# Performance work log

Measured on AMD Instinct MI355X. Metric: run time of the kernel, lower is better.

Reference implementation:

```python
import jax, jax.numpy as jnp
import numpy as np

D_MODEL = 1024
NUM_HEADS = 16
D_K = D_MODEL // NUM_HEADS
FFN_SIZE = 4096
EPS = 1e-6


def _layer_norm(x, gamma, beta):
    mu = jnp.mean(x, axis=-1, keepdims=True)
    var = jnp.var(x, axis=-1, keepdims=True)
    return (x - mu) / jnp.sqrt(var + EPS) * gamma + beta


def setup_inputs() -> dict:
    key = jax.random.key(0)
    ks = jax.random.split(key, 12)
    B, S = 2, 2048
    s_attn = 1.0 / np.sqrt(D_MODEL)
    s_ffn1 = 1.0 / np.sqrt(D_MODEL)
    s_ffn2 = 1.0 / np.sqrt(FFN_SIZE)
    return {
        "x": jax.random.normal(ks[0], (B, S, D_MODEL), dtype=jnp.float32),
        "W_q": jax.random.normal(ks[1], (D_MODEL, D_MODEL), dtype=jnp.float32) * s_attn,
        "W_k": jax.random.normal(ks[2], (D_MODEL, D_MODEL), dtype=jnp.float32) * s_attn,
        "W_v": jax.random.normal(ks[3], (D_MODEL, D_MODEL), dtype=jnp.float32) * s_attn,
        "W_o": jax.random.normal(ks[4], (D_MODEL, D_MODEL), dtype=jnp.float32) * s_attn,
        "b_o": jnp.zeros((D_MODEL,), dtype=jnp.float32),
        "W1": jax.random.normal(ks[5], (D_MODEL, FFN_SIZE), dtype=jnp.float32) * s_ffn1,
        "b1": jnp.zeros((FFN_SIZE,), dtype=jnp.float32),
        "W2": jax.random.normal(ks[6], (FFN_SIZE, D_MODEL), dtype=jnp.float32) * s_ffn2,
        "b2": jnp.zeros((D_MODEL,), dtype=jnp.float32),
        "ln1_g": jnp.ones((D_MODEL,), dtype=jnp.float32),
        "ln1_b": jnp.zeros((D_MODEL,), dtype=jnp.float32),
        "ln2_g": jnp.ones((D_MODEL,), dtype=jnp.float32),
        "ln2_b": jnp.zeros((D_MODEL,), dtype=jnp.float32),
    }


def reference(x, W_q, W_k, W_v, W_o, b_o, W1, b1, W2, b2,
              ln1_g, ln1_b, ln2_g, ln2_b):
    B, S, _ = x.shape

    # --- self-attention sublayer (pre-norm residual) ---
    h = _layer_norm(x, ln1_g, ln1_b)
    q = (h @ W_q).reshape(B, S, NUM_HEADS, D_K).transpose(0, 2, 1, 3)  # [B,H,S,Dk]
    k = (h @ W_k).reshape(B, S, NUM_HEADS, D_K).transpose(0, 2, 1, 3)
    v = (h @ W_v).reshape(B, S, NUM_HEADS, D_K).transpose(0, 2, 1, 3)
    scores = jnp.einsum("bhqd,bhkd->bhqk", q, k) / jnp.sqrt(jnp.float32(D_K))
    attn = jax.nn.softmax(scores, axis=-1)
    ctx = jnp.einsum("bhqk,bhkd->bhqd", attn, v)
    ctx = ctx.transpose(0, 2, 1, 3).reshape(B, S, D_MODEL)
    x = x + (ctx @ W_o + b_o)

    # --- FFN sublayer (pre-norm residual) ---
    h2 = _layer_norm(x, ln2_g, ln2_b)
    f = jax.nn.relu(h2 @ W1 + b1) @ W2 + b2
    return x + f
```

## Files before the change

kernel.cpp:

```cpp
#include <hip/hip_runtime.h>
#include <cstdint>
#include <cstddef>


typedef __attribute__((ext_vector_type(8))) __bf16 bf16x8;
typedef __attribute__((ext_vector_type(4))) __bf16 bf16x4;
typedef __attribute__((ext_vector_type(4))) float f32x4;

__device__ __forceinline__ void async16(const void* g, void* l) {
  __builtin_amdgcn_global_load_lds(
      (__attribute__((address_space(1))) void*)g,
      (__attribute__((address_space(3))) void*)l, 16, 0, 0);
}

__device__ __forceinline__ f32x4 mfma16(bf16x8 a, bf16x8 b, f32x4 c) {
  return __builtin_amdgcn_mfma_f32_16x16x32_bf16(a, b, c, 0, 0, 0);
}

template <int N>
__device__ __forceinline__ void wait_vmcnt() {
  if constexpr (N == 0) {
    asm volatile("s_waitcnt vmcnt(0)" ::: "memory");
  } else if constexpr (N == 3) {
    asm volatile("s_waitcnt vmcnt(3)" ::: "memory");
  } else {
    asm volatile("s_waitcnt vmcnt(4)" ::: "memory");
  }
}
__device__ __forceinline__ void barrier_raw() {
  asm volatile("s_barrier" ::: "memory");
}
__device__ __forceinline__ void lgkm0() {
  asm volatile("s_waitcnt lgkmcnt(0)" ::: "memory");
}

__global__ __launch_bounds__(256) void transpose_all(
    const float* __restrict__ Wq, const float* __restrict__ Wk,
    const float* __restrict__ Wv, const float* __restrict__ Wo,
    const float* __restrict__ W1, const float* __restrict__ W2,
    __bf16* __restrict__ WqkvT, __bf16* __restrict__ WoT,
    __bf16* __restrict__ W1T, __bf16* __restrict__ W2T) {
  const int id = blockIdx.x;
  const float* in;
  __bf16* out;
  int ld_in, ld_out, c0, r0;
  if (id < 1024) {
    const int which = id >> 8, tl = id & 255;
    c0 = (tl & 15) * 64;
    r0 = (tl >> 4) * 64;
    ld_in = 1024;
    ld_out = 1024;
    if (which == 0) { in = Wq; out = WqkvT; }
    else if (which == 1) { in = Wk; out = WqkvT + 1048576; }
    else if (which == 2) { in = Wv; out = WqkvT + 2097152; }
    else { in = Wo; out = WoT; }
  } else if (id < 2048) {
    const int tl = id - 1024;
    c0 = (tl & 63) * 64;
    r0 = (tl >> 6) * 64;
    in = W1; out = W1T; ld_in = 4096; ld_out = 1024;
  } else {
    const int tl = id - 2048;
    c0 = (tl & 15) * 64;
    r0 = (tl >> 4) * 64;
    in = W2; out = W2T; ld_in = 1024; ld_out = 4096;
  }
  __shared__ __bf16 tile[64][65];
  const int tx = threadIdx.x & 63, ty = threadIdx.x >> 6;
#pragma unroll
  for (int i = 0; i < 16; i++) {
    int r = ty + i * 4;
    tile[r][tx] = (__bf16)in[(size_t)(r0 + r) * ld_in + c0 + tx];
  }
  __syncthreads();
#pragma unroll
  for (int i = 0; i < 16; i++) {
    int r = ty + i * 4;
    out[(size_t)(c0 + r) * ld_out + r0 + tx] = tile[tx][r];
  }
}

__global__ __launch_bounds__(256) void transpose_vt_perm(
    const unsigned short* __restrict__ in, unsigned short* __restrict__ out,
    int ld_in, int ld_out) {
  __shared__ unsigned short tile[64][65];
  const int c0 = blockIdx.x * 64, r0 = blockIdx.y * 64;
  const int tx = threadIdx.x & 63, ty = threadIdx.x >> 6;
#pragma unroll
  for (int i = 0; i < 16; i++) {
    int r = ty + i * 4;
    tile[r][tx] = in[(size_t)(r0 + r) * ld_in + c0 + tx];
  }
  __syncthreads();
  const int ptx = (tx & 32) + 2 * (tx & 15) + ((tx >> 4) & 1);
#pragma unroll
  for (int i = 0; i < 16; i++) {
    int r = ty + i * 4;
    out[(size_t)(c0 + r) * ld_out + r0 + ptx] = tile[tx][r];
  }
}

__global__ __launch_bounds__(256) void ln_kernel(
    const float* __restrict__ xin, const float* __restrict__ g,
    const float* __restrict__ bt, __bf16* __restrict__ out) {
  const int tok = blockIdx.x * 4 + (threadIdx.x >> 6);
  const int lane = threadIdx.x & 63;
  const int base0 = lane * 8, base1 = 512 + lane * 8;
  const float* xr = xin + (size_t)tok * 1024;
  float v[16];
  float4 a0 = *(const float4*)(xr + base0);
  float4 a1 = *(const float4*)(xr + base0 + 4);
  float4 a2 = *(const float4*)(xr + base1);
  float4 a3 = *(const float4*)(xr + base1 + 4);
  v[0] = a0.x; v[1] = a0.y; v[2] = a0.z; v[3] = a0.w;
  v[4] = a1.x; v[5] = a1.y; v[6] = a1.z; v[7] = a1.w;
  v[8] = a2.x; v[9] = a2.y; v[10] = a2.z; v[11] = a2.w;
  v[12] = a3.x; v[13] = a3.y; v[14] = a3.z; v[15] = a3.w;
  float s = 0.f, s2 = 0.f;
#pragma unroll
  for (int i = 0; i < 16; i++) { s += v[i]; s2 += v[i] * v[i]; }
#pragma unroll
  for (int m = 1; m < 64; m <<= 1) {
    s += __shfl_xor(s, m);
    s2 += __shfl_xor(s2, m);
  }
  const float mean = s * (1.f / 1024.f);
  const float var = s2 * (1.f / 1024.f) - mean * mean;
  const float rstd = rsqrtf(var + 1e-6f);
  float4 g0 = *(const float4*)(g + base0), g1 = *(const float4*)(g + base0 + 4);
  float4 g2 = *(const float4*)(g + base1), g3 = *(const float4*)(g + base1 + 4);
  float4 b0 = *(const float4*)(bt + base0), b1v = *(const float4*)(bt + base0 + 4);
  float4 b2v = *(const float4*)(bt + base1), b3 = *(const float4*)(bt + base1 + 4);
  float gg[16] = {g0.x, g0.y, g0.z, g0.w, g1.x, g1.y, g1.z, g1.w,
                  g2.x, g2.y, g2.z, g2.w, g3.x, g3.y, g3.z, g3.w};
  float bb[16] = {b0.x, b0.y, b0.z, b0.w, b1v.x, b1v.y, b1v.z, b1v.w,
                  b2v.x, b2v.y, b2v.z, b2v.w, b3.x, b3.y, b3.z, b3.w};
  bf16x8 o0, o1;
#pragma unroll
  for (int j = 0; j < 8; j++) {
    o0[j] = (__bf16)((v[j] - mean) * rstd * gg[j] + bb[j]);
    o1[j] = (__bf16)((v[8 + j] - mean) * rstd * gg[8 + j] + bb[8 + j]);
  }
  __bf16* op = out + (size_t)tok * 1024;
  *(bf16x8*)(op + base0) = o0;
  *(bf16x8*)(op + base1) = o1;
}

template <int EPI, int SPLITS = 1>
__global__ __launch_bounds__(512, 2) void gemm256(
    const __bf16* __restrict__ A, int lda, const __bf16* __restrict__ BT,
    int ldb, void* __restrict__ C, int ldc, int Kb,
    const float* __restrict__ bias) {
  const int t = threadIdx.x;
  const int m0 = blockIdx.x * 256, n0 = blockIdx.y * 256;
  const int kz = (SPLITS > 1) ? blockIdx.z : 0;
  __shared__ __align__(16) __bf16 As[2][2][8192];
  __shared__ __align__(16) __bf16 Bs[2][2][8192];
  const int lane = t & 63;
  const int quad = lane >> 4, l15 = lane & 15;
  const int w = t >> 6, wm = w >> 2, wn = w & 3;

  f32x4 acc[8][4] = {};

  const int rr = t >> 3;
  const int ca = (t & 7) ^ (rr & 7);
  const int cc = rr & 31;
  const int wnb = t >> 8;
  const int cb = (t & 7) ^ (cc & 7);
  const __bf16* gA = A + (size_t)kz * Kb + (size_t)(m0 + rr) * lda + ca * 8;
  const __bf16* gB = BT + (size_t)kz * Kb +
                     (size_t)(n0 + wnb * 64 + cc) * ldb + cb * 8;
  const size_t a64 = (size_t)64 * lda, a128 = (size_t)128 * lda;
  const size_t b32 = (size_t)32 * ldb, b128 = (size_t)128 * ldb;

  auto stageA = [&](int buf, int mq, int ko) {
    const __bf16* g = gA + (mq ? a64 : 0) + ko;
    __bf16* l = &As[buf][mq][t * 8];
    async16(g, l);
    async16(g + a128, l + 4096);
  };
  auto stageB = [&](int buf, int nq, int ko) {
    const __bf16* g = gB + (nq ? b32 : 0) + ko;
    __bf16* l = &Bs[buf][nq][t * 8];
    async16(g, l);
    async16(g + b128, l + 4096);
  };

  const int arow = wm * 4096 + l15 * 64;
  const int brow = wn * 2048 + l15 * 64;
  const int x7 = l15 & 7;

  auto loadA = [&](int buf, int mq, bf16x8 (&af)[4][2]) {
#pragma unroll
    for (int mi = 0; mi < 4; mi++)
#pragma unroll
      for (int kk = 0; kk < 2; kk++)
        af[mi][kk] = *(const bf16x8*)&As[buf][mq]
            [arow + mi * 1024 + (((kk * 4 + quad) ^ x7) * 8)];
  };
  auto loadB = [&](int buf, int nq, bf16x8 (&bv)[2][2]) {
#pragma unroll
    for (int ni = 0; ni < 2; ni++)
#pragma unroll
      for (int kk = 0; kk < 2; kk++)
        bv[ni][kk] = *(const bf16x8*)&Bs[buf][nq]
            [brow + ni * 1024 + (((kk * 4 + quad) ^ x7) * 8)];
  };
  auto mm = [&](int mq, int nq, const bf16x8 (&af)[4][2],
                const bf16x8 (&bv)[2][2]) {
    __builtin_amdgcn_s_setprio(1);
#pragma unroll
    for (int mi = 0; mi < 4; mi++)
#pragma unroll
      for (int ni = 0; ni < 2; ni++)
#pragma unroll
        for (int kk = 0; kk < 2; kk++)
          acc[mq * 4 + mi][nq * 2 + ni] =
              mfma16(af[mi][kk], bv[ni][kk], acc[mq * 4 + mi][nq * 2 + ni]);
    __builtin_amdgcn_s_setprio(0);
  };

  const int NT = Kb / 64;
  stageA(0, 0, 0); stageB(0, 0, 0); stageA(0, 1, 0); stageB(0, 1, 0);
  stageA(1, 0, 64); stageB(1, 0, 64);
  wait_vmcnt<4>();
  barrier_raw();

  bf16x8 af[4][2], b0[2][2], b1[2][2];
  for (int s = 0; s < NT; ++s) {
    const int buf = s & 1;
    const int ko1 = (s + 1) * 64, ko2 = (s + 2) * 64;
    loadA(buf, 0, af);
    loadB(buf, 0, b0);
    if (s + 1 < NT) stageA(buf ^ 1, 1, ko1);
    barrier_raw();
    lgkm0();
    mm(0, 0, af, b0);
    barrier_raw();
    loadB(buf, 1, b1);
    if (s + 1 < NT) stageB(buf ^ 1, 1, ko1);
    barrier_raw();
    lgkm0();
    mm(0, 1, af, b1);
    barrier_raw();
    loadA(buf, 1, af);
    if (s + 2 < NT) stageA(buf, 0, ko2);
    barrier_raw();
    lgkm0();
    mm(1, 0, af, b0);
    barrier_raw();
    if (s + 2 < NT) {
      stageB(buf, 0, ko2);
      wait_vmcnt<4>();
    } else {
      wait_vmcnt<0>();
    }
    barrier_raw();
    mm(1, 1, af, b1);
    barrier_raw();
  }

  float biasv[4];
  if constexpr (EPI == 2) {
#pragma unroll
    for (int ni = 0; ni < 4; ni++)
      biasv[ni] = bias[n0 + wn * 64 + ni * 16 + l15];
  }
  __bf16* Cb = (__bf16*)C;
  if constexpr (SPLITS > 1)
    Cb += (size_t)kz * (size_t)gridDim.x * 256 * ldc;
#pragma unroll
  for (int mi = 0; mi < 8; mi++)
#pragma unroll
    for (int ni = 0; ni < 4; ni++)
#pragma unroll
      for (int r = 0; r < 4; r++) {
        const int row = m0 + wm * 128 + mi * 16 + quad * 4 + r;
        const int col = n0 + wn * 64 + ni * 16 + l15;
        float v = acc[mi][ni][r];
        if constexpr (EPI == 0) {
          Cb[(size_t)row * ldc + col] = (__bf16)v;
        } else {
          v += biasv[ni];
          Cb[(size_t)row * ldc + col] = (__bf16)fmaxf(v, 0.f);
        }
      }
}

template <int EPI, int TM, int SPLITS = 1>
__global__ __launch_bounds__(256) void gemm_bt(
    const __bf16* __restrict__ A, int lda, const __bf16* __restrict__ BT,
    int ldb, void* __restrict__ C, int ldc, int Kb,
    const float* __restrict__ bias, const float* __restrict__ res, int ldres) {
  const int t = threadIdx.x;
  const int m0 = blockIdx.x * TM, n0 = blockIdx.y * 128;
  const int kz = (SPLITS > 1) ? blockIdx.z : 0;
  __shared__ __align__(16) __bf16 As[3][TM * 32];
  __shared__ __align__(16) __bf16 Bs[3][128 * 32];
  const int lane = t & 63, w = t >> 6;
  const int quad = lane >> 4, l15 = lane & 15;
  const int wm = w >> 1, wn = w & 1;
  constexpr int MF = TM / 32;
  constexpr int LOADS = TM / 64 + 2;

  f32x4 acc[MF][4] = {};

  const int swc = ((t & 3) ^ ((t >> 3) & 3)) * 8;
  const __bf16* ga = A + (size_t)(m0 + (t >> 2)) * lda + swc + (size_t)kz * Kb;
  const __bf16* gb = BT + (size_t)(n0 + (t >> 2)) * ldb + swc + (size_t)kz * Kb;
  const size_t a64 = (size_t)64 * lda, b64 = (size_t)64 * ldb;

  auto stage = [&](int buf) {
#pragma unroll
    for (int i = 0; i < TM / 64; i++)
      async16(ga + i * a64, As[buf] + t * 8 + i * 2048);
    async16(gb, Bs[buf] + t * 8);
    async16(gb + b64, Bs[buf] + t * 8 + 2048);
    ga += 32;
    gb += 32;
  };
  const int ce = (quad ^ ((l15 >> 1) & 3)) * 8;
  auto compute = [&](int buf) {
    bf16x8 af[MF], bfr[4];
#pragma unroll
    for (int i = 0; i < MF; i++)
      af[i] = *(const bf16x8*)&As[buf][(wm * (TM / 2) + i * 16 + l15) * 32 + ce];
#pragma unroll
    for (int i = 0; i < 4; i++)
      bfr[i] = *(const bf16x8*)&Bs[buf][(wn * 64 + i * 16 + l15) * 32 + ce];
#pragma unroll
    for (int mi = 0; mi < MF; mi++)
#pragma unroll
      for (int ni = 0; ni < 4; ni++)
        acc[mi][ni] = mfma16(af[mi], bfr[ni], acc[mi][ni]);
  };

  const int iters = Kb / 32;
  stage(0);
  stage(1);
  int cur = 0, stg = 2;
  for (int it = 0; it < iters - 1; ++it) {
    wait_vmcnt<LOADS>();
    barrier_raw();
    if (it + 2 < iters) stage(stg);
    compute(cur);
    cur = (cur == 2) ? 0 : cur + 1;
    stg = (stg == 2) ? 0 : stg + 1;
  }
  wait_vmcnt<0>();
  barrier_raw();
  compute(cur);

  float biasv[4];
  if constexpr (EPI != 0) {
#pragma unroll
    for (int ni = 0; ni < 4; ni++)
      biasv[ni] = bias[n0 + wn * 64 + ni * 16 + l15];
  }
  __bf16* Cb = (__bf16*)C;
  if constexpr (SPLITS > 1)
    Cb += (size_t)kz * gridDim.x * TM * ldc;
#pragma unroll
  for (int mi = 0; mi < MF; mi++)
#pragma unroll
    for (int ni = 0; ni < 4; ni++)
#pragma unroll
      for (int r = 0; r < 4; r++) {
        const int row = m0 + wm * (TM / 2) + mi * 16 + quad * 4 + r;
        const int col = n0 + wn * 64 + ni * 16 + l15;
        float v = acc[mi][ni][r];
        if constexpr (EPI == 0) {
          Cb[(size_t)row * ldc + col] = (__bf16)v;
        } else if constexpr (EPI == 1) {
          v += biasv[ni] + res[(size_t)row * ldres + col];
          ((float*)C)[(size_t)row * ldc + col] = v;
        } else {
          v += biasv[ni];
          ((__bf16*)C)[(size_t)row * ldc + col] = (__bf16)fmaxf(v, 0.f);
        }
      }
}

__global__ __launch_bounds__(256) void reduce_split4(
    const __bf16* __restrict__ P, const float* __restrict__ bias,
    const float* __restrict__ res, float* __restrict__ out) {
  const int row = blockIdx.x, c = threadIdx.x * 4;
  const size_t i = (size_t)row * 1024 + c;
  float4 r = *(const float4*)(res + i);
  float4 bv = *(const float4*)(bias + c);
  float s0 = r.x + bv.x, s1 = r.y + bv.y, s2 = r.z + bv.z, s3 = r.w + bv.w;
#pragma unroll
  for (int j = 0; j < 4; j++) {
    bf16x4 p = *(const bf16x4*)(P + (size_t)j * 4194304 + i);
    s0 += (float)p[0];
    s1 += (float)p[1];
    s2 += (float)p[2];
    s3 += (float)p[3];
  }
  float4 o = {s0, s1, s2, s3};
  *(float4*)(out + i) = o;
}

__global__ __launch_bounds__(256, 2) void attn_kernel(
    const __bf16* __restrict__ QKV, const __bf16* __restrict__ VT,
    __bf16* __restrict__ ctx) {
  const int qt = blockIdx.x, bh = blockIdx.y;
  const int b = bh >> 4, h = bh & 15;
  const int t = threadIdx.x, w = t >> 6, lane = t & 63;
  const int quad = lane >> 4, l15 = lane & 15;
  const int tok0 = b * 2048;
  const int q0w = tok0 + qt * 128 + w * 32;

  __shared__ __align__(16) __bf16 Ks[2][128 * 64];
  __shared__ __align__(16) __bf16 VTs[2][64 * 128];

  const float qs = 0.18033688011112042f;
  bf16x8 qf[2][2];
#pragma unroll
  for (int mi = 0; mi < 2; mi++)
#pragma unroll
    for (int kb = 0; kb < 2; kb++) {
      const __bf16* src = QKV + (size_t)(q0w + mi * 16 + l15) * 3072 + h * 64 +
                          kb * 32 + quad * 8;
      bf16x8 r = *(const bf16x8*)src;
#pragma unroll
      for (int j = 0; j < 8; j++) r[j] = (__bf16)((float)r[j] * qs);
      qf[mi][kb] = r;
    }

  f32x4 lacc[2] = {};
  f32x4 O[2][4] = {};

  const int krow = t >> 3;
  const int kcg = (((t & 7) ^ (krow & 7)) * 8);
  const int vrow = t >> 4;
  const int vcg = (((2 * (t & 15)) ^ ((vrow & 7) * 2)) * 4);
  const int x7 = l15 & 7;

  auto stage = [&](int buf, int kt) {
    const int ktok = tok0 + kt * 128;
#pragma unroll
    for (int j = 0; j < 4; j++) {
      const __bf16* gp =
          QKV + (size_t)(ktok + krow + j * 32) * 3072 + 1024 + h * 64 + kcg;
      async16(gp, Ks[buf] + t * 8 + j * 2048);
    }
#pragma unroll
    for (int j = 0; j < 4; j++) {
      const __bf16* gp =
          VT + (size_t)(h * 64 + vrow + j * 16) * 4096 + ktok + vcg;
      async16(gp, VTs[buf] + t * 8 + j * 2048);
    }
  };

  stage(0, 0);
  wait_vmcnt<0>();
  barrier_raw();

  int buf = 0;
  for (int kt = 0; kt < 16; ++kt) {
    if (kt + 1 < 16) stage(buf ^ 1, kt + 1);

    f32x4 sT[2][8];
    __builtin_amdgcn_s_setprio(1);
#pragma unroll
    for (int kt8 = 0; kt8 < 8; kt8++) {
      f32x4 a0 = {}, a1 = {};
#pragma unroll
      for (int kb = 0; kb < 2; kb++) {
        bf16x8 kf = *(const bf16x8*)&Ks[buf][(kt8 * 16 + l15) * 64 +
                                            (((kb * 4 + quad) ^ x7) * 8)];
        a0 = mfma16(kf, qf[0][kb], a0);
        a1 = mfma16(kf, qf[1][kb], a1);
      }
      sT[0][kt8] = a0;
      sT[1][kt8] = a1;
    }
    __builtin_amdgcn_s_setprio(0);

#pragma unroll
    for (int kb = 0; kb < 4; kb++) {
      bf16x8 pf0, pf1;
#pragma unroll
      for (int hf = 0; hf < 2; hf++)
#pragma unroll
        for (int r = 0; r < 4; r++) {
          const float p0 = __builtin_amdgcn_exp2f(sT[0][2 * kb + hf][r]);
          const float p1 = __builtin_amdgcn_exp2f(sT[1][2 * kb + hf][r]);
          lacc[0][r] += p0;
          lacc[1][r] += p1;
          pf0[r * 2 + hf] = (__bf16)p0;
          pf1[r * 2 + hf] = (__bf16)p1;
        }
      __builtin_amdgcn_s_setprio(1);
#pragma unroll
      for (int nd = 0; nd < 4; nd++) {
        bf16x8 vf = *(const bf16x8*)&VTs[buf][(nd * 16 + l15) * 128 +
                                             (((4 * kb + quad) ^ x7) * 8)];
        O[0][nd] = mfma16(pf0, vf, O[0][nd]);
        O[1][nd] = mfma16(pf1, vf, O[1][nd]);
      }
      __builtin_amdgcn_s_setprio(0);
    }

    wait_vmcnt<0>();
    barrier_raw();
    buf ^= 1;
  }

#pragma unroll
  for (int mi = 0; mi < 2; mi++) {
    float lsum = lacc[mi][0] + lacc[mi][1] + lacc[mi][2] + lacc[mi][3];
    lsum += __shfl_xor(lsum, 16);
    lsum += __shfl_xor(lsum, 32);
    float rl[4];
#pragma unroll
    for (int r = 0; r < 4; r++) rl[r] = 1.0f / __shfl(lsum, quad * 4 + r);
#pragma unroll
    for (int nd = 0; nd < 4; nd++)
#pragma unroll
      for (int r = 0; r < 4; r++) {
        const int tokq = q0w + mi * 16 + quad * 4 + r;
        const int col = h * 64 + nd * 16 + l15;
        ctx[(size_t)tokq * 1024 + col] = (__bf16)(O[mi][nd][r] * rl[r]);
      }
  }
}

extern "C" void kernel_launch(void* const* d_in, const int* in_sizes, int n_in,
                              void* d_out, int out_size, void* d_ws,
                              size_t ws_size, hipStream_t stream) {
  (void)in_sizes; (void)n_in; (void)out_size; (void)ws_size;

  const float* x = (const float*)d_in[0];
  const float* Wq = (const float*)d_in[1];
  const float* Wk = (const float*)d_in[2];
  const float* Wv = (const float*)d_in[3];
  const float* Wo = (const float*)d_in[4];
  const float* b_o = (const float*)d_in[5];
  const float* W1 = (const float*)d_in[6];
  const float* b1 = (const float*)d_in[7];
  const float* W2 = (const float*)d_in[8];
  const float* b2 = (const float*)d_in[9];
  const float* ln1g = (const float*)d_in[10];
  const float* ln1b = (const float*)d_in[11];
  const float* ln2g = (const float*)d_in[12];
  const float* ln2b = (const float*)d_in[13];

  char* ws = (char*)d_ws;
  __bf16* h = (__bf16*)(ws + 0);
  __bf16* W1T = (__bf16*)(ws + 8388608);
  __bf16* WqkvT = (__bf16*)(ws + 16777216);
  __bf16* WoT = (__bf16*)(ws + 23068672);
  __bf16* QKV = (__bf16*)(ws + 25165824);
  __bf16* VT = (__bf16*)(ws + 50331648);
  __bf16* ctx = (__bf16*)(ws + 58720256);
  __bf16* f1 = (__bf16*)(ws + 33554432);
  __bf16* Pw2 = (__bf16*)(ws + 0);
  float* x1 = (float*)(ws + 67108864);
  __bf16* W2T = (__bf16*)(ws + 83886080);

  const dim3 blk(256);
  const dim3 blk512(512);

  transpose_all<<<dim3(3072), blk, 0, stream>>>(Wq, Wk, Wv, Wo, W1, W2, WqkvT,
                                                WoT, W1T, W2T);

  ln_kernel<<<dim3(1024), blk, 0, stream>>>(x, ln1g, ln1b, h);

  gemm256<0><<<dim3(16, 12), blk512, 0, stream>>>(
      h, 1024, WqkvT, 1024, (void*)QKV, 3072, 1024, nullptr);

  transpose_vt_perm<<<dim3(16, 64), blk, 0, stream>>>(
      (const unsigned short*)(QKV + 2048), (unsigned short*)VT, 3072, 4096);

  attn_kernel<<<dim3(16, 32), blk, 0, stream>>>(QKV, VT, ctx);

  gemm_bt<1, 64><<<dim3(64, 8), blk, 0, stream>>>(
      ctx, 1024, WoT, 1024, (void*)x1, 1024, 1024, b_o, x, 1024);

  ln_kernel<<<dim3(1024), blk, 0, stream>>>(x1, ln2g, ln2b, h);

  gemm256<2><<<dim3(16, 16), blk512, 0, stream>>>(
      h, 1024, W1T, 1024, (void*)f1, 4096, 1024, b1);

  gemm256<0, 4><<<dim3(16, 4, 4), blk512, 0, stream>>>(
      f1, 4096, W2T, 4096, (void*)Pw2, 1024, 1024, nullptr);
  reduce_split4<<<dim3(4096), blk, 0, stream>>>(Pw2, b2, x1, (float*)d_out);
}
```

Baseline: 313.8 us.

## Shrink attention tiles to 64 queries and keys, remap blocks by head group

Each attention block now covers 64 query rows instead of 128, with 16 rows per wave, and streams K/V in 64-key tiles over 32 iterations. The grid doubles to 1024 one-dimensional blocks, with a remapping that groups heads into sets of 8×4, and launch bounds are raised to allow 4 blocks per CU. The aim is more waves in flight and better load balance across CUs, plus better cache locality for K/V shared across query tiles. In exchange, each wave reuses the loaded K/V tiles for half as many queries, so LDS traffic and the number of barriers per unit of work go up.

```diff
diff --git a/kernel.cpp b/kernel.cpp
--- a/kernel.cpp
+++ b/kernel.cpp
@@ -401,54 +401,53 @@
   *(float4*)(out + i) = o;
 }
 
-__global__ __launch_bounds__(256, 2) void attn_kernel(
+__global__ __launch_bounds__(256, 4) void attn_kernel(
     const __bf16* __restrict__ QKV, const __bf16* __restrict__ VT,
     __bf16* __restrict__ ctx) {
-  const int qt = blockIdx.x, bh = blockIdx.y;
+  const int id = blockIdx.x;
+  const int xg = id & 7, idx = id >> 3;
+  const int bh = xg * 4 + (idx & 3);
+  const int qt = idx >> 2;
   const int b = bh >> 4, h = bh & 15;
   const int t = threadIdx.x, w = t >> 6, lane = t & 63;
   const int quad = lane >> 4, l15 = lane & 15;
   const int tok0 = b * 2048;
-  const int q0w = tok0 + qt * 128 + w * 32;
-
-  __shared__ __align__(16) __bf16 Ks[2][128 * 64];
-  __shared__ __align__(16) __bf16 VTs[2][64 * 128];
+  const int q0w = tok0 + qt * 64 + w * 16;
+
+  __shared__ __align__(16) __bf16 Ks[2][64 * 64];
+  __shared__ __align__(16) __bf16 VTs[2][64 * 64];
 
   const float qs = 0.18033688011112042f;
-  bf16x8 qf[2][2];
-#pragma unroll
-  for (int mi = 0; mi < 2; mi++)
-#pragma unroll
-    for (int kb = 0; kb < 2; kb++) {
-      const __bf16* src = QKV + (size_t)(q0w + mi * 16 + l15) * 3072 + h * 64 +
-                          kb * 32 + quad * 8;
-      bf16x8 r = *(const bf16x8*)src;
-#pragma unroll
-      for (int j = 0; j < 8; j++) r[j] = (__bf16)((float)r[j] * qs);
-      qf[mi][kb] = r;
-    }
-
-  f32x4 lacc[2] = {};
-  f32x4 O[2][4] = {};
-
-  const int krow = t >> 3;
-  const int kcg = (((t & 7) ^ (krow & 7)) * 8);
-  const int vrow = t >> 4;
-  const int vcg = (((2 * (t & 15)) ^ ((vrow & 7) * 2)) * 4);
+  bf16x8 qf[2];
+#pragma unroll
+  for (int kb = 0; kb < 2; kb++) {
+    const __bf16* src =
+        QKV + (size_t)(q0w + l15) * 3072 + h * 64 + kb * 32 + quad * 8;
+    bf16x8 r = *(const bf16x8*)src;
+#pragma unroll
+    for (int j = 0; j < 8; j++) r[j] = (__bf16)((float)r[j] * qs);
+    qf[kb] = r;
+  }
+
+  f32x4 lacc = {};
+  f32x4 O[4] = {};
+
+  const int srow = t >> 3;
+  const int sc = ((t & 7) ^ (srow & 7)) * 8;
   const int x7 = l15 & 7;
 
   auto stage = [&](int buf, int kt) {
-    const int ktok = tok0 + kt * 128;
-#pragma unroll
-    for (int j = 0; j < 4; j++) {
+    const int ktok = tok0 + kt * 64;
+#pragma unroll
+    for (int j = 0; j < 2; j++) {
       const __bf16* gp =
-          QKV + (size_t)(ktok + krow + j * 32) * 3072 + 1024 + h * 64 + kcg;
+          QKV + (size_t)(ktok + srow + j * 32) * 3072 + 1024 + h * 64 + sc;
       async16(gp, Ks[buf] + t * 8 + j * 2048);
     }
 #pragma unroll
-    for (int j = 0; j < 4; j++) {
+    for (int j = 0; j < 2; j++) {
       const __bf16* gp =
-          VT + (size_t)(h * 64 + vrow + j * 16) * 4096 + ktok + vcg;
+          VT + (size_t)(h * 64 + srow + j * 32) * 4096 + ktok + sc;
       async16(gp, VTs[buf] + t * 8 + j * 2048);
     }
   };
@@ -458,47 +457,41 @@
   barrier_raw();
 
   int buf = 0;
-  for (int kt = 0; kt < 16; ++kt) {
-    if (kt + 1 < 16) stage(buf ^ 1, kt + 1);
-
-    f32x4 sT[2][8];
+  for (int kt = 0; kt < 32; ++kt) {
+    if (kt + 1 < 32) stage(buf ^ 1, kt + 1);
+
+    f32x4 sT[4];
     __builtin_amdgcn_s_setprio(1);
 #pragma unroll
-    for (int kt8 = 0; kt8 < 8; kt8++) {
-      f32x4 a0 = {}, a1 = {};
+    for (int kt8 = 0; kt8 < 4; kt8++) {
+      f32x4 a = {};
 #pragma unroll
       for (int kb = 0; kb < 2; kb++) {
         bf16x8 kf = *(const bf16x8*)&Ks[buf][(kt8 * 16 + l15) * 64 +
                                             (((kb * 4 + quad) ^ x7) * 8)];
-        a0 = mfma16(kf, qf[0][kb], a0);
-        a1 = mfma16(kf, qf[1][kb], a1);
+        a = mfma16(kf, qf[kb], a);
       }
-      sT[0][kt8] = a0;
-      sT[1][kt8] = a1;
+      sT[kt8] = a;
     }
     __builtin_amdgcn_s_setprio(0);
 
 #pragma unroll
-    for (int kb = 0; kb < 4; kb++) {
-      bf16x8 pf0, pf1;
+    for (int kb = 0; kb < 2; kb++) {
+      bf16x8 pf;
 #pragma unroll
       for (int hf = 0; hf < 2; hf++)
 #pragma unroll
         for (int r = 0; r < 4; r++) {
-          const float p0 = __builtin_amdgcn_exp2f(sT[0][2 * kb + hf][r]);
-          const float p1 = __builtin_amdgcn_exp2f(sT[1][2 * kb + hf][r]);
-          lacc[0][r] += p0;
-          lacc[1][r] += p1;
-          pf0[r * 2 + hf] = (__bf16)p0;
-          pf1[r * 2 + hf] = (__bf16)p1;
+          const float p = __builtin_amdgcn_exp2f(sT[2 * kb + hf][r]);
+          lacc[r] += p;
+          pf[r * 2 + hf] = (__bf16)p;
         }
       __builtin_amdgcn_s_setprio(1);
 #pragma unroll
       for (int nd = 0; nd < 4; nd++) {
-        bf16x8 vf = *(const bf16x8*)&VTs[buf][(nd * 16 + l15) * 128 +
-                                             (((4 * kb + quad) ^ x7) * 8)];
-        O[0][nd] = mfma16(pf0, vf, O[0][nd]);
-        O[1][nd] = mfma16(pf1, vf, O[1][nd]);
+        bf16x8 vf = *(const bf16x8*)&VTs[buf][(nd * 16 + l15) * 64 +
+                                             (((kb * 4 + quad) ^ x7) * 8)];
+        O[nd] = mfma16(pf, vf, O[nd]);
       }
       __builtin_amdgcn_s_setprio(0);
     }
@@ -508,23 +501,20 @@
     buf ^= 1;
   }
 
-#pragma unroll
-  for (int mi = 0; mi < 2; mi++) {
-    float lsum = lacc[mi][0] + lacc[mi][1] + lacc[mi][2] + lacc[mi][3];
-    lsum += __shfl_xor(lsum, 16);
-    lsum += __shfl_xor(lsum, 32);
-    float rl[4];
-#pragma unroll
-    for (int r = 0; r < 4; r++) rl[r] = 1.0f / __shfl(lsum, quad * 4 + r);
-#pragma unroll
-    for (int nd = 0; nd < 4; nd++)
-#pragma unroll
-      for (int r = 0; r < 4; r++) {
-        const int tokq = q0w + mi * 16 + quad * 4 + r;
-        const int col = h * 64 + nd * 16 + l15;
-        ctx[(size_t)tokq * 1024 + col] = (__bf16)(O[mi][nd][r] * rl[r]);
-      }
-  }
+  float lsum = lacc[0] + lacc[1] + lacc[2] + lacc[3];
+  lsum += __shfl_xor(lsum, 16);
+  lsum += __shfl_xor(lsum, 32);
+  float rl[4];
+#pragma unroll
+  for (int r = 0; r < 4; r++) rl[r] = 1.0f / __shfl(lsum, quad * 4 + r);
+#pragma unroll
+  for (int nd = 0; nd < 4; nd++)
+#pragma unroll
+    for (int r = 0; r < 4; r++) {
+      const int tokq = q0w + quad * 4 + r;
+      const int col = h * 64 + nd * 16 + l15;
+      ctx[(size_t)tokq * 1024 + col] = (__bf16)(O[nd][r] * rl[r]);
+    }
 }
 
 extern "C" void kernel_launch(void* const* d_in, const int* in_sizes, int n_in,
@@ -574,7 +564,7 @@
   transpose_vt_perm<<<dim3(16, 64), blk, 0, stream>>>(
       (const unsigned short*)(QKV + 2048), (unsigned short*)VT, 3072, 4096);
 
-  attn_kernel<<<dim3(16, 32), blk, 0, stream>>>(QKV, VT, ctx);
+  attn_kernel<<<dim3(1024), blk, 0, stream>>>(QKV, VT, ctx);
 
   gemm_bt<1, 64><<<dim3(64, 8), blk, 0, stream>>>(
       ctx, 1024, WoT, 1024, (void*)x1, 1024, 1024, b_o, x, 1024);
```

Measured after the change: 321.2 us. 1.02x slower.

## Triple-buffer attention K/V tiles with 64-key steps and XCD-aware block mapping

Applied to the files above, without the earlier changes.

The attention kernel's K/V stage shrinks from 128 keys to 64 keys and moves from double to triple buffering in shared memory. Two tiles load ahead, and the kernel waits with a partial vmcnt so loads overlap compute, with one barrier per iteration. The grid becomes 1D, and block ids are remapped so consecutive ids land on different XCDs while each XCD works on a small group of heads, which should improve L2 reuse of K/V. Smaller tiles mean more loop iterations and barriers, but less shared memory per block.

```diff
diff --git a/kernel.cpp b/kernel.cpp
--- a/kernel.cpp
+++ b/kernel.cpp
@@ -404,15 +404,18 @@
 __global__ __launch_bounds__(256, 2) void attn_kernel(
     const __bf16* __restrict__ QKV, const __bf16* __restrict__ VT,
     __bf16* __restrict__ ctx) {
-  const int qt = blockIdx.x, bh = blockIdx.y;
+  const int id = blockIdx.x;
+  const int xg = id & 7, idx = id >> 3;
+  const int bh = xg * 4 + (idx & 3);
+  const int qt = idx >> 2;
   const int b = bh >> 4, h = bh & 15;
   const int t = threadIdx.x, w = t >> 6, lane = t & 63;
   const int quad = lane >> 4, l15 = lane & 15;
   const int tok0 = b * 2048;
   const int q0w = tok0 + qt * 128 + w * 32;
 
-  __shared__ __align__(16) __bf16 Ks[2][128 * 64];
-  __shared__ __align__(16) __bf16 VTs[2][64 * 128];
+  __shared__ __align__(16) __bf16 Ks[3][64 * 64];
+  __shared__ __align__(16) __bf16 VTs[3][64 * 64];
 
   const float qs = 0.18033688011112042f;
   bf16x8 qf[2][2];
@@ -431,40 +434,31 @@
   f32x4 lacc[2] = {};
   f32x4 O[2][4] = {};
 
-  const int krow = t >> 3;
-  const int kcg = (((t & 7) ^ (krow & 7)) * 8);
-  const int vrow = t >> 4;
-  const int vcg = (((2 * (t & 15)) ^ ((vrow & 7) * 2)) * 4);
+  const int srow = t >> 3;
+  const int sc = ((t & 7) ^ (srow & 7)) * 8;
   const int x7 = l15 & 7;
 
   auto stage = [&](int buf, int kt) {
-    const int ktok = tok0 + kt * 128;
-#pragma unroll
-    for (int j = 0; j < 4; j++) {
+    const int ktok = tok0 + kt * 64;
+#pragma unroll
+    for (int j = 0; j < 2; j++) {
       const __bf16* gp =
-          QKV + (size_t)(ktok + krow + j * 32) * 3072 + 1024 + h * 64 + kcg;
+          QKV + (size_t)(ktok + srow + j * 32) * 3072 + 1024 + h * 64 + sc;
       async16(gp, Ks[buf] + t * 8 + j * 2048);
     }
 #pragma unroll
-    for (int j = 0; j < 4; j++) {
+    for (int j = 0; j < 2; j++) {
       const __bf16* gp =
-          VT + (size_t)(h * 64 + vrow + j * 16) * 4096 + ktok + vcg;
+          VT + (size_t)(h * 64 + srow + j * 32) * 4096 + ktok + sc;
       async16(gp, VTs[buf] + t * 8 + j * 2048);
     }
   };
 
-  stage(0, 0);
-  wait_vmcnt<0>();
-  barrier_raw();
-
-  int buf = 0;
-  for (int kt = 0; kt < 16; ++kt) {
-    if (kt + 1 < 16) stage(buf ^ 1, kt + 1);
-
-    f32x4 sT[2][8];
+  auto compute = [&](int buf) {
+    f32x4 sT[2][4];
     __builtin_amdgcn_s_setprio(1);
 #pragma unroll
-    for (int kt8 = 0; kt8 < 8; kt8++) {
+    for (int kt8 = 0; kt8 < 4; kt8++) {
       f32x4 a0 = {}, a1 = {};
 #pragma unroll
       for (int kb = 0; kb < 2; kb++) {
@@ -479,7 +473,7 @@
     __builtin_amdgcn_s_setprio(0);
 
 #pragma unroll
-    for (int kb = 0; kb < 4; kb++) {
+    for (int kb = 0; kb < 2; kb++) {
       bf16x8 pf0, pf1;
 #pragma unroll
       for (int hf = 0; hf < 2; hf++)
@@ -495,18 +489,29 @@
       __builtin_amdgcn_s_setprio(1);
 #pragma unroll
       for (int nd = 0; nd < 4; nd++) {
-        bf16x8 vf = *(const bf16x8*)&VTs[buf][(nd * 16 + l15) * 128 +
-                                             (((4 * kb + quad) ^ x7) * 8)];
+        bf16x8 vf = *(const bf16x8*)&VTs[buf][(nd * 16 + l15) * 64 +
+                                             (((kb * 4 + quad) ^ x7) * 8)];
         O[0][nd] = mfma16(pf0, vf, O[0][nd]);
         O[1][nd] = mfma16(pf1, vf, O[1][nd]);
       }
       __builtin_amdgcn_s_setprio(0);
     }
-
-    wait_vmcnt<0>();
-    barrier_raw();
-    buf ^= 1;
-  }
+  };
+
+  stage(0, 0);
+  stage(1, 1);
+  int cur = 0, stg = 2;
+  for (int it = 0; it < 31; ++it) {
+    wait_vmcnt<4>();
+    barrier_raw();
+    if (it + 2 < 32) stage(stg, it + 2);
+    compute(cur);
+    cur = (cur == 2) ? 0 : cur + 1;
+    stg = (stg == 2) ? 0 : stg + 1;
+  }
+  wait_vmcnt<0>();
+  barrier_raw();
+  compute(cur);
 
 #pragma unroll
   for (int mi = 0; mi < 2; mi++) {
@@ -574,7 +579,7 @@
   transpose_vt_perm<<<dim3(16, 64), blk, 0, stream>>>(
       (const unsigned short*)(QKV + 2048), (unsigned short*)VT, 3072, 4096);
 
-  attn_kernel<<<dim3(16, 32), blk, 0, stream>>>(QKV, VT, ctx);
+  attn_kernel<<<dim3(512), blk, 0, stream>>>(QKV, VT, ctx);
 
   gemm_bt<1, 64><<<dim3(64, 8), blk, 0, stream>>>(
       ctx, 1024, WoT, 1024, (void*)x1, 1024, 1024, b_o, x, 1024);
```

New measurement: 312.3 us. No clear change (-0.5%).
